# Kernel optimization log

Hardware: AMD Instinct MI355X
Metric: run time of the kernel (lower is better)

## Reference

```python
import jax, jax.numpy as jnp
import numpy as np

EPS = 1e-5


def grid_sample_bilinear(feat, grid):
    """torch.nn.functional.grid_sample, mode='bilinear', padding_mode='zeros',
    align_corners=False.  feat: [N,C,H,W], grid: [N,P,1,2] in [-1,1] -> [N,C,P,1]."""
    N, C, H, W = feat.shape
    x = grid[..., 0]
    y = grid[..., 1]                                # [N,P,1]
    ix = ((x + 1.0) * W - 1.0) * 0.5
    iy = ((y + 1.0) * H - 1.0) * 0.5
    ix0 = jnp.floor(ix)
    iy0 = jnp.floor(iy)
    wx1 = ix - ix0
    wy1 = iy - iy0
    flat = feat.reshape(N, C, H * W)

    def corner(iy_, ix_, w):
        valid = (ix_ >= 0) & (ix_ <= W - 1) & (iy_ >= 0) & (iy_ <= H - 1)
        idx = (jnp.clip(iy_, 0, H - 1) * W + jnp.clip(ix_, 0, W - 1)).astype(jnp.int32)
        v = jnp.take_along_axis(flat, idx.reshape(N, 1, -1), axis=2)
        v = v.reshape(N, C, idx.shape[1], idx.shape[2])
        return v * (w * valid.astype(feat.dtype))[:, None]

    return (corner(iy0, ix0, (1.0 - wy1) * (1.0 - wx1))
            + corner(iy0, ix0 + 1.0, (1.0 - wy1) * wx1)
            + corner(iy0 + 1.0, ix0, wy1 * (1.0 - wx1))
            + corner(iy0 + 1.0, ix0 + 1.0, wy1 * wx1))


def _feature_sampling(mlvl_feats, reference_points, pc_range, img_shape, lidar2img):
    ref3d = reference_points
    # denormalize reference points into the point-cloud range
    xyz = reference_points * (pc_range[3:6] - pc_range[0:3]) + pc_range[0:3]  # [B,Q,3]
    B, nq = xyz.shape[:2]
    num_cam = lidar2img.shape[1]
    pts = jnp.concatenate([xyz, jnp.ones_like(xyz[..., :1])], axis=-1)        # [B,Q,4]
    # project to each camera: [B,cam,Q,4]
    cam = jnp.einsum('bnij,bqj->bnqi', lidar2img, pts)
    z = cam[..., 2:3]
    mask = z > EPS
    xy = cam[..., 0:2] / jnp.maximum(z, EPS)
    xy = xy / jnp.stack([img_shape[1], img_shape[0]])  # x/W, y/H
    xy = (xy - 0.5) * 2.0                               # to [-1,1]
    mask = (mask & (xy[..., 0:1] > -1.0) & (xy[..., 0:1] < 1.0)
                 & (xy[..., 1:2] > -1.0) & (xy[..., 1:2] < 1.0))
    mask = mask.reshape(B, num_cam, 1, nq, 1, 1).transpose(0, 2, 3, 1, 4, 5)
    mask = mask.astype(jnp.float32)
    grid = xy.reshape(B * num_cam, nq, 1, 2)
    sampled = []
    for feat in mlvl_feats:
        _, N, C, H, W = feat.shape
        s = grid_sample_bilinear(feat.reshape(B * N, C, H, W), grid)  # [B*N,C,Q,1]
        s = s.reshape(B, N, C, nq, 1).transpose(0, 2, 3, 1, 4)        # [B,C,Q,N,1]
        sampled.append(s)
    sampled_feats = jnp.stack(sampled, axis=-1)  # [B,C,Q,cam,1,n_levels]
    return ref3d, sampled_feats, mask


def setup_inputs() -> dict:
    key = jax.random.key(0)
    ks = jax.random.split(key, 8)
    B, NC, C = 1, 6, 256
    sizes = [(116, 200), (58, 100), (29, 50), (15, 25)]
    feats = [jax.random.normal(ks[i], (B, NC, C, h, w), dtype=jnp.float32)
             for i, (h, w) in enumerate(sizes)]
    reference_points = jax.random.uniform(ks[4], (B, 900, 3), dtype=jnp.float32)
    pc_range = jnp.array([-51.2, -51.2, -5.0, 51.2, 51.2, 3.0], dtype=jnp.float32)
    img_shape = jnp.array([928.0, 1600.0], dtype=jnp.float32)  # (H, W)
    lidar2img = jax.random.normal(ks[5], (B, NC, 4, 4), dtype=jnp.float32) * 100.0
    return {"mlvl_feats1": feats[0], "mlvl_feats2": feats[1],
            "mlvl_feats3": feats[2], "mlvl_feats4": feats[3],
            "reference_points": reference_points, "pc_range": pc_range,
            "img_shape": img_shape, "lidar2img": lidar2img}


def reference(mlvl_feats1, mlvl_feats2, mlvl_feats3, mlvl_feats4,
              reference_points, pc_range, img_shape, lidar2img):
    return _feature_sampling([mlvl_feats1, mlvl_feats2, mlvl_feats3, mlvl_feats4],
                             reference_points, pc_range, img_shape, lidar2img)
```

## Files before the change

kernel.cpp:

```cpp
#include <hip/hip_runtime.h>

#define EPS_F 1e-5f

__global__ __launch_bounds__(256) void fs_kernel(
    const float* __restrict__ f0, const float* __restrict__ f1,
    const float* __restrict__ f2, const float* __restrict__ f3,
    const float* __restrict__ ref_pts, const float* __restrict__ pc_range,
    const float* __restrict__ img_shape, const float* __restrict__ l2i,
    float* __restrict__ out)
{
    const int bid = blockIdx.x;
    const int n = bid % 6;
    const int q = bid / 6;
    const int c = threadIdx.x;

    const float X = ref_pts[q * 3 + 0] * (pc_range[3] - pc_range[0]) + pc_range[0];
    const float Y = ref_pts[q * 3 + 1] * (pc_range[4] - pc_range[1]) + pc_range[1];
    const float Z = ref_pts[q * 3 + 2] * (pc_range[5] - pc_range[2]) + pc_range[2];
    const float* M = l2i + n * 16;
    const float cx = M[0] * X + M[1] * Y + M[2]  * Z + M[3];
    const float cy = M[4] * X + M[5] * Y + M[6]  * Z + M[7];
    const float cz = M[8] * X + M[9] * Y + M[10] * Z + M[11];
    const float denom = fmaxf(cz, EPS_F);
    const float u = (cx / denom) / img_shape[1];
    const float v = (cy / denom) / img_shape[0];
    const float xn = (u - 0.5f) * 2.0f;
    const float yn = (v - 0.5f) * 2.0f;

    if (threadIdx.x == 0) {
        const bool m = (cz > EPS_F) && (xn > -1.0f) && (xn < 1.0f)
                                    && (yn > -1.0f) && (yn < 1.0f);
        out[5532300 + q * 6 + n] = m ? 1.0f : 0.0f;
    }
    if (n == 0 && threadIdx.x < 3) {
        out[q * 3 + threadIdx.x] = ref_pts[q * 3 + threadIdx.x];
    }

    const float* const feats[4] = {f0, f1, f2, f3};
    const int Hs[4] = {116, 58, 29, 15};
    const int Ws[4] = {200, 100, 50, 25};

    float acc[4];
    #pragma unroll
    for (int l = 0; l < 4; ++l) {
        const int W = Ws[l];
        const int H = Hs[l];
        const float ix = ((xn + 1.0f) * (float)W - 1.0f) * 0.5f;
        const float iy = ((yn + 1.0f) * (float)H - 1.0f) * 0.5f;
        const float ix0f = floorf(ix);
        const float iy0f = floorf(iy);
        const float wx1 = ix - ix0f, wx0 = 1.0f - wx1;
        const float wy1 = iy - iy0f, wy0 = 1.0f - wy1;
        const bool vx0 = (ix0f >= 0.0f)  && (ix0f <= (float)(W - 1));
        const bool vx1 = (ix0f >= -1.0f) && (ix0f <= (float)(W - 2));
        const bool vy0 = (iy0f >= 0.0f)  && (iy0f <= (float)(H - 1));
        const bool vy1 = (iy0f >= -1.0f) && (iy0f <= (float)(H - 2));

        float val = 0.0f;
        if ((vx0 || vx1) && (vy0 || vy1)) {
            const int x0 = (int)ix0f;
            const int x1 = x0 + 1;
            const float* base = feats[l] + (size_t)(n * 256 + c) * (size_t)(H * W);
            if (vy0) {
                const float* row = base + (int)iy0f * W;
                float r = 0.0f;
                if (vx0) r += wx0 * row[x0];
                if (vx1) r += wx1 * row[x1];
                val += wy0 * r;
            }
            if (vy1) {
                const float* row = base + ((int)iy0f + 1) * W;
                float r = 0.0f;
                if (vx0) r += wx0 * row[x0];
                if (vx1) r += wx1 * row[x1];
                val += wy1 * r;
            }
        }
        acc[l] = val;
    }

    float4 o;
    o.x = acc[0]; o.y = acc[1]; o.z = acc[2]; o.w = acc[3];
    *(float4*)(out + 2700 + (size_t)c * 21600 + q * 24 + n * 4) = o;
}

extern "C" void kernel_launch(void* const* d_in, const int* in_sizes, int n_in,
                              void* d_out, int out_size, void* d_ws, size_t ws_size,
                              hipStream_t stream) {
    const float* f0  = (const float*)d_in[0];
    const float* f1  = (const float*)d_in[1];
    const float* f2  = (const float*)d_in[2];
    const float* f3  = (const float*)d_in[3];
    const float* rp  = (const float*)d_in[4];
    const float* pcr = (const float*)d_in[5];
    const float* ish = (const float*)d_in[6];
    const float* l2i = (const float*)d_in[7];
    float* out = (float*)d_out;

    fs_kernel<<<5400, 256, 0, stream>>>(f0, f1, f2, f3, rp, pcr, ish, l2i, out);
}
```

Before: 239.4 us.

## Process all six cameras per block with branchless clamped bilinear gathers

```diff
diff --git a/kernel.cpp b/kernel.cpp
--- a/kernel.cpp
+++ b/kernel.cpp
@@ -9,79 +9,104 @@
     const float* __restrict__ img_shape, const float* __restrict__ l2i,
     float* __restrict__ out)
 {
-    const int bid = blockIdx.x;
-    const int n = bid % 6;
-    const int q = bid / 6;
+    const int q = blockIdx.x;
     const int c = threadIdx.x;
 
     const float X = ref_pts[q * 3 + 0] * (pc_range[3] - pc_range[0]) + pc_range[0];
     const float Y = ref_pts[q * 3 + 1] * (pc_range[4] - pc_range[1]) + pc_range[1];
     const float Z = ref_pts[q * 3 + 2] * (pc_range[5] - pc_range[2]) + pc_range[2];
-    const float* M = l2i + n * 16;
-    const float cx = M[0] * X + M[1] * Y + M[2]  * Z + M[3];
-    const float cy = M[4] * X + M[5] * Y + M[6]  * Z + M[7];
-    const float cz = M[8] * X + M[9] * Y + M[10] * Z + M[11];
-    const float denom = fmaxf(cz, EPS_F);
-    const float u = (cx / denom) / img_shape[1];
-    const float v = (cy / denom) / img_shape[0];
-    const float xn = (u - 0.5f) * 2.0f;
-    const float yn = (v - 0.5f) * 2.0f;
+    const float ish0 = img_shape[0];
+    const float ish1 = img_shape[1];
 
-    if (threadIdx.x == 0) {
+    float xn_a[6], yn_a[6];
+    unsigned mbits = 0u;
+    #pragma unroll
+    for (int n = 0; n < 6; ++n) {
+        const float* M = l2i + n * 16;
+        const float cx = M[0] * X + M[1] * Y + M[2]  * Z + M[3];
+        const float cy = M[4] * X + M[5] * Y + M[6]  * Z + M[7];
+        const float cz = M[8] * X + M[9] * Y + M[10] * Z + M[11];
+        const float denom = fmaxf(cz, EPS_F);
+        const float u = (cx / denom) / ish1;
+        const float v = (cy / denom) / ish0;
+        const float xn = (u - 0.5f) * 2.0f;
+        const float yn = (v - 0.5f) * 2.0f;
+        xn_a[n] = xn;
+        yn_a[n] = yn;
         const bool m = (cz > EPS_F) && (xn > -1.0f) && (xn < 1.0f)
                                     && (yn > -1.0f) && (yn < 1.0f);
-        out[5532300 + q * 6 + n] = m ? 1.0f : 0.0f;
+        mbits |= (m ? 1u : 0u) << n;
     }
-    if (n == 0 && threadIdx.x < 3) {
-        out[q * 3 + threadIdx.x] = ref_pts[q * 3 + threadIdx.x];
+
+    if (c < 6) {
+        out[5532300 + q * 6 + c] = ((mbits >> c) & 1u) ? 1.0f : 0.0f;
+    }
+    if (c < 3) {
+        out[q * 3 + c] = ref_pts[q * 3 + c];
     }
 
     const float* const feats[4] = {f0, f1, f2, f3};
     const int Hs[4] = {116, 58, 29, 15};
     const int Ws[4] = {200, 100, 50, 25};
 
-    float acc[4];
+    float* const obase = out + 2700 + (size_t)c * 21600 + q * 24;
+
     #pragma unroll
-    for (int l = 0; l < 4; ++l) {
-        const int W = Ws[l];
-        const int H = Hs[l];
-        const float ix = ((xn + 1.0f) * (float)W - 1.0f) * 0.5f;
-        const float iy = ((yn + 1.0f) * (float)H - 1.0f) * 0.5f;
-        const float ix0f = floorf(ix);
-        const float iy0f = floorf(iy);
-        const float wx1 = ix - ix0f, wx0 = 1.0f - wx1;
-        const float wy1 = iy - iy0f, wy0 = 1.0f - wy1;
-        const bool vx0 = (ix0f >= 0.0f)  && (ix0f <= (float)(W - 1));
-        const bool vx1 = (ix0f >= -1.0f) && (ix0f <= (float)(W - 2));
-        const bool vy0 = (iy0f >= 0.0f)  && (iy0f <= (float)(H - 1));
-        const bool vy1 = (iy0f >= -1.0f) && (iy0f <= (float)(H - 2));
+    for (int n = 0; n < 6; ++n) {
+        const float xn = xn_a[n];
+        const float yn = yn_a[n];
 
-        float val = 0.0f;
-        if ((vx0 || vx1) && (vy0 || vy1)) {
-            const int x0 = (int)ix0f;
-            const int x1 = x0 + 1;
-            const float* base = feats[l] + (size_t)(n * 256 + c) * (size_t)(H * W);
-            if (vy0) {
-                const float* row = base + (int)iy0f * W;
-                float r = 0.0f;
-                if (vx0) r += wx0 * row[x0];
-                if (vx1) r += wx1 * row[x1];
-                val += wy0 * r;
+        const float ix3  = ((xn + 1.0f) * 25.0f - 1.0f) * 0.5f;
+        const float iy3  = ((yn + 1.0f) * 15.0f - 1.0f) * 0.5f;
+        const float ix3f = floorf(ix3);
+        const float iy3f = floorf(iy3);
+        const bool cam_valid = (ix3f >= -1.0f) && (ix3f <= 24.0f)
+                            && (iy3f >= -1.0f) && (iy3f <= 14.0f);
+
+        float acc0 = 0.0f, acc1 = 0.0f, acc2 = 0.0f, acc3 = 0.0f;
+        if (cam_valid) {
+            float accl[4];
+            #pragma unroll
+            for (int l = 0; l < 4; ++l) {
+                const int W = Ws[l];
+                const int H = Hs[l];
+                const float ix = ((xn + 1.0f) * (float)W - 1.0f) * 0.5f;
+                const float iy = ((yn + 1.0f) * (float)H - 1.0f) * 0.5f;
+                const float ix0f = floorf(ix);
+                const float iy0f = floorf(iy);
+                const float wx1 = ix - ix0f, wx0 = 1.0f - wx1;
+                const float wy1 = iy - iy0f, wy0 = 1.0f - wy1;
+                const bool vx0 = (ix0f >= 0.0f)  && (ix0f <= (float)(W - 1));
+                const bool vx1 = (ix0f >= -1.0f) && (ix0f <= (float)(W - 2));
+                const bool vy0 = (iy0f >= 0.0f)  && (iy0f <= (float)(H - 1));
+                const bool vy1 = (iy0f >= -1.0f) && (iy0f <= (float)(H - 2));
+
+                const float w00 = (vy0 && vx0) ? wy0 * wx0 : 0.0f;
+                const float w01 = (vy0 && vx1) ? wy0 * wx1 : 0.0f;
+                const float w10 = (vy1 && vx0) ? wy1 * wx0 : 0.0f;
+                const float w11 = (vy1 && vx1) ? wy1 * wx1 : 0.0f;
+
+                const int x0 = (int)fminf(fmaxf(ix0f,        0.0f), (float)(W - 1));
+                const int x1 = (int)fminf(fmaxf(ix0f + 1.0f, 0.0f), (float)(W - 1));
+                const int y0 = (int)fminf(fmaxf(iy0f,        0.0f), (float)(H - 1));
+                const int y1 = (int)fminf(fmaxf(iy0f + 1.0f, 0.0f), (float)(H - 1));
+
+                const float* base = feats[l] + (size_t)(n * 256 + c) * (size_t)(H * W);
+                const float* r0 = base + y0 * W;
+                const float* r1 = base + y1 * W;
+                const float v00 = r0[x0];
+                const float v01 = r0[x1];
+                const float v10 = r1[x0];
+                const float v11 = r1[x1];
+                accl[l] = w00 * v00 + w01 * v01 + w10 * v10 + w11 * v11;
             }
-            if (vy1) {
-                const float* row = base + ((int)iy0f + 1) * W;
-                float r = 0.0f;
-                if (vx0) r += wx0 * row[x0];
-                if (vx1) r += wx1 * row[x1];
-                val += wy1 * r;
-            }
+            acc0 = accl[0]; acc1 = accl[1]; acc2 = accl[2]; acc3 = accl[3];
         }
-        acc[l] = val;
+
+        float4 o;
+        o.x = acc0; o.y = acc1; o.z = acc2; o.w = acc3;
+        *(float4*)(obase + n * 4) = o;
     }
-
-    float4 o;
-    o.x = acc[0]; o.y = acc[1]; o.z = acc[2]; o.w = acc[3];
-    *(float4*)(out + 2700 + (size_t)c * 21600 + q * 24 + n * 4) = o;
 }
 
 extern "C" void kernel_launch(void* const* d_in, const int* in_sizes, int n_in,
@@ -97,5 +122,5 @@
     const float* l2i = (const float*)d_in[7];
     float* out = (float*)d_out;
 
-    fs_kernel<<<5400, 256, 0, stream>>>(f0, f1, f2, f3, rp, pcr, ish, l2i, out);
+    fs_kernel<<<900, 256, 0, stream>>>(f0, f1, f2, f3, rp, pcr, ish, l2i, out);
 }
```

After: 250.6 us. 4.6% more time.
